# Optimization experiments

Measured on AMD Instinct MI355X. Metric: run time of the kernel, lower is better.

The kernel has to match this reference:

```python
import jax, jax.numpy as jnp
import numpy as np

BASE_C = 0.001
T = 0.7
MIN_RATIO = 0.5
MAX_RATIO = 2.0
EPS = 1e-7
BATCH, IN_DIM, HID, OUT_DIM = 65536, 784, 128, 10
WEIGHT_STD = 0.02


def _mobius_add(u, v, c):
    # (u +_c v) on the Poincare ball, last-dim vectors
    uv = jnp.sum(u * v, axis=-1, keepdims=True)
    uu = jnp.sum(u * u, axis=-1, keepdims=True)
    vv = jnp.sum(v * v, axis=-1, keepdims=True)
    num = (1.0 + 2.0 * c * uv + c * vv) * u + (1.0 - c * uu) * v
    den = 1.0 + 2.0 * c * uv + (c * c) * uu * vv
    return num / jnp.maximum(den, EPS)


def _mobius_scalar(x, c, r):
    # r (x)_c : tanh(r * artanh(sqrt(c)||x||)) * x / (sqrt(c)||x||)
    n = jnp.sqrt(jnp.maximum(jnp.sum(x * x, axis=-1, keepdims=True), EPS * EPS))
    sc = jnp.sqrt(c)
    arg = jnp.clip(sc * n, EPS, 1.0 - 1e-5)
    return jnp.tanh(r * jnp.arctanh(arg)) * x / (sc * n)


def poincare_ball_layer(h, u, c, t):
    # hyperbolic interpolation: ((1-t) (x)_c h) (+)_c (t (x)_c u)
    return _mobius_add(_mobius_scalar(h, c, 1.0 - t), _mobius_scalar(u, c, t), c)


def setup_inputs() -> dict:
    key = jax.random.key(0)
    ks = jax.random.split(key, 4)
    x = jax.random.normal(ks[0], (BATCH, IN_DIM), dtype=jnp.float32)
    weights1 = WEIGHT_STD * jax.random.normal(ks[1], (IN_DIM, HID), dtype=jnp.float32)
    bias1 = jnp.zeros((HID,), dtype=jnp.float32)
    weights2 = WEIGHT_STD * jax.random.normal(ks[2], (HID, HID), dtype=jnp.float32)
    bias2 = jnp.zeros((HID,), dtype=jnp.float32)
    out_weights = WEIGHT_STD * jax.random.normal(ks[3], (HID, OUT_DIM), dtype=jnp.float32)
    out_bias = jnp.zeros((OUT_DIM,), dtype=jnp.float32)
    curvature_scale = jnp.ones((1,), dtype=jnp.float32)
    return {"x": x, "weights1": weights1, "bias1": bias1, "weights2": weights2,
            "bias2": bias2, "out_weights": out_weights, "out_bias": out_bias,
            "curvature_scale": curvature_scale}


def reference(x, weights1, bias1, weights2, bias2, out_weights, out_bias, curvature_scale):
    x_flat = x.reshape(x.shape[0], -1)
    h = jnp.tanh(x_flat @ weights1 + bias1)            # [B, HID]
    u = jax.nn.sigmoid(h @ weights2 + bias2)           # [B, HID]
    # torch uses .item() -> curvature scale is detached from autodiff
    s = jax.lax.stop_gradient(jax.nn.sigmoid(curvature_scale[0]))
    adaptive_c = BASE_C * (MIN_RATIO + (MAX_RATIO - MIN_RATIO) * s)
    z = poincare_ball_layer(h, u, adaptive_c, T)
    z = jnp.where(jnp.any(jnp.isnan(z)), h, z)         # NaN fallback
    return z @ out_weights + out_bias
```

## Files before the change

kernel.cpp:

```cpp
#include <hip/hip_runtime.h>

typedef __attribute__((ext_vector_type(8))) short short8;
typedef __attribute__((ext_vector_type(4))) short short4v;
typedef __attribute__((ext_vector_type(4))) float f32x4;

#define BATCH 65536
#define IN_DIM 784
#define HID 128
#define OUT_DIM 10
#define KPAD 800
#define NKS 25
#define BM 128
#define NBLK (BATCH / BM)

#define OFF_W1H 0
#define OFF_W1L 204800
#define OFF_W2S 409600
#define OFF_W3S 442368

__device__ __forceinline__ unsigned short bf16_rne(float f) {
    unsigned u = __float_as_uint(f);
    return (unsigned short)((u + 0x7FFFu + ((u >> 16) & 1u)) >> 16);
}
__device__ __forceinline__ float fast_tanh(float x) {
    float e = __expf(2.0f * x);
    return 1.0f - 2.0f / (e + 1.0f);
}

__global__ void prep_kernel(const float* __restrict__ W1, const float* __restrict__ W2,
                            const float* __restrict__ W3,
                            unsigned short* __restrict__ w1h, unsigned short* __restrict__ w1l,
                            unsigned short* __restrict__ w2s, unsigned short* __restrict__ w3s) {
    int b = blockIdx.x, t = threadIdx.x;
    if (b < HID) {
        int col = b;
        for (int k = t; k < KPAD; k += 256) {
            float v = (k < IN_DIM) ? W1[k * HID + col] : 0.0f;
            unsigned u = __float_as_uint(v);
            unsigned short hi = (unsigned short)(u >> 16);
            float hif = __uint_as_float(u & 0xFFFF0000u);
            unsigned short lo = bf16_rne(v - hif);
            int idx = ((k >> 5) * HID + col) * 32 + (k & 31);
            w1h[idx] = hi; w1l[idx] = lo;
        }
    } else if (b == HID) {
        for (int i = t; i < HID * HID; i += 256) {
            int n = i >> 7, k = i & 127;
            w2s[i] = bf16_rne(W2[k * HID + n]);
        }
    } else {
        for (int i = t; i < 16 * HID; i += 256) {
            int j = i >> 7, k = i & 127;
            float v = (j < OUT_DIM) ? W3[k * OUT_DIM + j] : 0.0f;
            w3s[i] = bf16_rne(v);
        }
    }
}

__launch_bounds__(256, 2)
__global__ void fused_kernel(const float* __restrict__ X,
                             const float* __restrict__ b1,
                             const float* __restrict__ b2,
                             const float* __restrict__ ob,
                             const float* __restrict__ csc,
                             const unsigned short* __restrict__ w1h,
                             const unsigned short* __restrict__ w1l,
                             const unsigned short* __restrict__ w2s,
                             const unsigned short* __restrict__ w3s,
                             float* __restrict__ OUT) {
    __shared__ unsigned short smem[2][2][HID][40];
    unsigned short (*ht)[136] = (unsigned short (*)[136])&smem[0][0][0][0];

    const int t = threadIdx.x;
    const int wid = t >> 6, lane = t & 63;
    const int lg = lane >> 4, lr = lane & 15;
    const int row0 = blockIdx.x * BM;

    f32x4 acc[2][8];
    #pragma unroll
    for (int f = 0; f < 8; ++f) {
        float bv = b1[16 * f + lr];
        f32x4 v = {bv, bv, bv, bv};
        acc[0][f] = v; acc[1][f] = v;
    }

    f32x4 xcur[2][2], xnxt[2][2];
    short8 wcur[4], wnxt[4];

    #define LOADX(dst, ks)                                                        \
        {                                                                         \
            int k0_ = (ks) * 32 + 8 * lg;                                         \
            _Pragma("unroll")                                                     \
            for (int rf = 0; rf < 2; ++rf) {                                      \
                f32x4 a_ = {0,0,0,0}, b_ = {0,0,0,0};                             \
                if (k0_ < IN_DIM) {                                               \
                    const f32x4* p_ = (const f32x4*)(X +                          \
                        (size_t)(row0 + wid * 32 + rf * 16 + lr) * IN_DIM + k0_); \
                    a_ = p_[0]; b_ = p_[1];                                       \
                }                                                                 \
                dst[rf][0] = a_; dst[rf][1] = b_;                                 \
            }                                                                     \
        }
    #define LOADW(dst, ks)                                                        \
        {                                                                         \
            const short8* ph_ = (const short8*)(w1h + (ks) * 4096) + t * 2;       \
            const short8* pl_ = (const short8*)(w1l + (ks) * 4096) + t * 2;       \
            dst[0] = ph_[0]; dst[1] = ph_[1];                                     \
            dst[2] = pl_[0]; dst[3] = pl_[1];                                     \
        }

    LOADX(xcur, 0);
    LOADW(wcur, 0);

    for (int ks = 0; ks < NKS; ++ks) {
        const int cur = ks & 1;
        {
            short8* dh = (short8*)&smem[cur][0][t >> 1][(t & 1) * 16];
            short8* dl = (short8*)&smem[cur][1][t >> 1][(t & 1) * 16];
            dh[0] = wcur[0]; dh[1] = wcur[1];
            dl[0] = wcur[2]; dl[1] = wcur[3];
        }
        if (ks + 1 < NKS) {
            LOADX(xnxt, ks + 1);
            LOADW(wnxt, ks + 1);
        }
        __syncthreads();

        short8 xh[2], xl[2];
        #pragma unroll
        for (int rf = 0; rf < 2; ++rf) {
            short8 h8, l8;
            #pragma unroll
            for (int j = 0; j < 8; ++j) {
                float v = (j < 4) ? xcur[rf][0][j] : xcur[rf][1][j - 4];
                unsigned u = __float_as_uint(v);
                h8[j] = (short)(u >> 16);
                float lof = v - __uint_as_float(u & 0xFFFF0000u);
                l8[j] = (short)(__float_as_uint(lof) >> 16);
            }
            xh[rf] = h8; xl[rf] = l8;
        }
        #pragma unroll
        for (int f = 0; f < 8; ++f) {
            const short8 bh = *(const short8*)&smem[cur][0][16 * f + lr][8 * lg];
            const short8 bl = *(const short8*)&smem[cur][1][16 * f + lr][8 * lg];
            acc[0][f] = __builtin_amdgcn_mfma_f32_16x16x32_bf16(xh[0], bh, acc[0][f], 0, 0, 0);
            acc[1][f] = __builtin_amdgcn_mfma_f32_16x16x32_bf16(xh[1], bh, acc[1][f], 0, 0, 0);
            acc[0][f] = __builtin_amdgcn_mfma_f32_16x16x32_bf16(xl[0], bh, acc[0][f], 0, 0, 0);
            acc[1][f] = __builtin_amdgcn_mfma_f32_16x16x32_bf16(xl[1], bh, acc[1][f], 0, 0, 0);
            acc[0][f] = __builtin_amdgcn_mfma_f32_16x16x32_bf16(xh[0], bl, acc[0][f], 0, 0, 0);
            acc[1][f] = __builtin_amdgcn_mfma_f32_16x16x32_bf16(xh[1], bl, acc[1][f], 0, 0, 0);
        }
        #pragma unroll
        for (int rf = 0; rf < 2; ++rf) { xcur[rf][0] = xnxt[rf][0]; xcur[rf][1] = xnxt[rf][1]; }
        #pragma unroll
        for (int j = 0; j < 4; ++j) wcur[j] = wnxt[j];
    }
    __syncthreads();

    const float cs = csc[0];
    const float sgc = 1.0f / (1.0f + __expf(-cs));
    const float c = 0.001f * (0.5f + 1.5f * sgc);
    const float sc = sqrtf(c);

    #pragma unroll
    for (int rf = 0; rf < 2; ++rf) {
        const int rbase = wid * 32 + rf * 16 + 4 * lg;
        #pragma unroll
        for (int f = 0; f < 8; ++f) {
            short4v pk;
            #pragma unroll
            for (int r = 0; r < 4; ++r) {
                float h = fast_tanh(acc[rf][f][r]);
                acc[rf][f][r] = h;
                pk[r] = (short)bf16_rne(h);
            }
            *(short4v*)(&ht[16 * f + lr][rbase]) = pk;
        }
    }

    f32x4 uacc[2][8];
    #pragma unroll
    for (int f = 0; f < 8; ++f) {
        float bv = b2[16 * f + lr];
        f32x4 v = {bv, bv, bv, bv};
        uacc[0][f] = v; uacc[1][f] = v;
    }
    #pragma unroll
    for (int ks2 = 0; ks2 < 4; ++ks2) {
        short8 a2[2];
        #pragma unroll
        for (int rf = 0; rf < 2; ++rf) {
            const int rbl = wid * 32 + rf * 16 + lr;
            #pragma unroll
            for (int i = 0; i < 8; ++i)
                a2[rf][i] = (short)ht[ks2 * 32 + 8 * lg + i][rbl];
        }
        #pragma unroll
        for (int f = 0; f < 8; ++f) {
            const short8 bb = *(const short8*)(w2s + (16 * f + lr) * HID + ks2 * 32 + 8 * lg);
            uacc[0][f] = __builtin_amdgcn_mfma_f32_16x16x32_bf16(a2[0], bb, uacc[0][f], 0, 0, 0);
            uacc[1][f] = __builtin_amdgcn_mfma_f32_16x16x32_bf16(a2[1], bb, uacc[1][f], 0, 0, 0);
        }
    }
    #pragma unroll
    for (int rf = 0; rf < 2; ++rf)
        #pragma unroll
        for (int f = 0; f < 8; ++f)
            #pragma unroll
            for (int r = 0; r < 4; ++r)
                uacc[rf][f][r] = 1.0f / (1.0f + __expf(-uacc[rf][f][r]));

    float cA[2][4], cB[2][4];
    #pragma unroll
    for (int rf = 0; rf < 2; ++rf) {
        float hh[4] = {0,0,0,0}, uu[4] = {0,0,0,0}, hu[4] = {0,0,0,0};
        #pragma unroll
        for (int f = 0; f < 8; ++f)
            #pragma unroll
            for (int r = 0; r < 4; ++r) {
                float h = acc[rf][f][r], u = uacc[rf][f][r];
                hh[r] += h * h; uu[r] += u * u; hu[r] += h * u;
            }
        #pragma unroll
        for (int m = 1; m <= 8; m <<= 1)
            #pragma unroll
            for (int r = 0; r < 4; ++r) {
                hh[r] += __shfl_xor(hh[r], m);
                uu[r] += __shfl_xor(uu[r], m);
                hu[r] += __shfl_xor(hu[r], m);
            }
        #pragma unroll
        for (int r = 0; r < 4; ++r) {
            float nh = sqrtf(fmaxf(hh[r], 1e-14f));
            float nu = sqrtf(fmaxf(uu[r], 1e-14f));
            float argh = fminf(fmaxf(sc * nh, 1e-7f), 1.0f - 1e-5f);
            float argu = fminf(fmaxf(sc * nu, 1e-7f), 1.0f - 1e-5f);
            float ath = 0.5f * __logf((1.0f + argh) / (1.0f - argh));
            float atu = 0.5f * __logf((1.0f + argu) / (1.0f - argu));
            float alpha = fast_tanh(0.3f * ath) / (sc * nh);
            float beta  = fast_tanh(0.7f * atu) / (sc * nu);
            float UV = alpha * beta * hu[r];
            float UU = alpha * alpha * hh[r];
            float VV = beta * beta * uu[r];
            float den = fmaxf(1.0f + 2.0f * c * UV + c * c * UU * VV, 1e-7f);
            cA[rf][r] = (1.0f + 2.0f * c * UV + c * VV) * alpha / den;
            cB[rf][r] = (1.0f - c * UU) * beta / den;
        }
    }
    #pragma unroll
    for (int rf = 0; rf < 2; ++rf) {
        const int rbase = wid * 32 + rf * 16 + 4 * lg;
        #pragma unroll
        for (int f = 0; f < 8; ++f) {
            short4v pk;
            #pragma unroll
            for (int r = 0; r < 4; ++r) {
                float z = cA[rf][r] * acc[rf][f][r] + cB[rf][r] * uacc[rf][f][r];
                pk[r] = (short)bf16_rne(z);
            }
            *(short4v*)(&ht[16 * f + lr][rbase]) = pk;
        }
    }

    float obv = (lr < OUT_DIM) ? ob[lr] : 0.0f;
    f32x4 oacc[2];
    oacc[0][0] = obv; oacc[0][1] = obv; oacc[0][2] = obv; oacc[0][3] = obv;
    oacc[1] = oacc[0];
    #pragma unroll
    for (int ks2 = 0; ks2 < 4; ++ks2) {
        short8 a3[2];
        #pragma unroll
        for (int rf = 0; rf < 2; ++rf) {
            const int rbl = wid * 32 + rf * 16 + lr;
            #pragma unroll
            for (int i = 0; i < 8; ++i)
                a3[rf][i] = (short)ht[ks2 * 32 + 8 * lg + i][rbl];
        }
        const short8 b3 = *(const short8*)(w3s + lr * HID + ks2 * 32 + 8 * lg);
        oacc[0] = __builtin_amdgcn_mfma_f32_16x16x32_bf16(a3[0], b3, oacc[0], 0, 0, 0);
        oacc[1] = __builtin_amdgcn_mfma_f32_16x16x32_bf16(a3[1], b3, oacc[1], 0, 0, 0);
    }
    if (lr < OUT_DIM) {
        #pragma unroll
        for (int rf = 0; rf < 2; ++rf) {
            const int rbase = row0 + wid * 32 + rf * 16 + 4 * lg;
            #pragma unroll
            for (int r = 0; r < 4; ++r)
                OUT[(size_t)(rbase + r) * OUT_DIM + lr] = oacc[rf][r];
        }
    }
}

extern "C" void kernel_launch(void* const* d_in, const int* in_sizes, int n_in,
                              void* d_out, int out_size, void* d_ws, size_t ws_size,
                              hipStream_t stream) {
    const float* X  = (const float*)d_in[0];
    const float* W1 = (const float*)d_in[1];
    const float* B1 = (const float*)d_in[2];
    const float* W2 = (const float*)d_in[3];
    const float* B2 = (const float*)d_in[4];
    const float* W3 = (const float*)d_in[5];
    const float* OB = (const float*)d_in[6];
    const float* CS = (const float*)d_in[7];
    unsigned short* w1h = (unsigned short*)((char*)d_ws + OFF_W1H);
    unsigned short* w1l = (unsigned short*)((char*)d_ws + OFF_W1L);
    unsigned short* w2s = (unsigned short*)((char*)d_ws + OFF_W2S);
    unsigned short* w3s = (unsigned short*)((char*)d_ws + OFF_W3S);
    prep_kernel<<<HID + 2, 256, 0, stream>>>(W1, W2, W3, w1h, w1l, w2s, w3s);
    fused_kernel<<<NBLK, 256, 0, stream>>>(X, B1, B2, OB, CS, w1h, w1l, w2s, w3s, (float*)d_out);
}
```

Before: 327.5 us.

## Read W1 fragments directly from global memory instead of staging through LDS

Drops the double-buffered LDS staging of the split bf16 W1 tiles and the per-step block barrier. Each wave now loads its MFMA B fragments straight from global memory, which relies on L1/L2 caching of the small shared weight matrix. LDS use shrinks to the post-GEMM buffer and launch bounds are raised to three blocks per CU for more occupancy. The cost is more global/L1 traffic per wave, weight loads no longer prefetched one step ahead, and tighter register limits that could cause spills.

```diff
diff --git a/kernel.cpp b/kernel.cpp
--- a/kernel.cpp
+++ b/kernel.cpp
@@ -57,7 +57,7 @@
     }
 }
 
-__launch_bounds__(256, 2)
+__launch_bounds__(256, 3)
 __global__ void fused_kernel(const float* __restrict__ X,
                              const float* __restrict__ b1,
                              const float* __restrict__ b2,
@@ -68,8 +68,7 @@
                              const unsigned short* __restrict__ w2s,
                              const unsigned short* __restrict__ w3s,
                              float* __restrict__ OUT) {
-    __shared__ unsigned short smem[2][2][HID][40];
-    unsigned short (*ht)[136] = (unsigned short (*)[136])&smem[0][0][0][0];
+    __shared__ unsigned short ht[HID][136];
 
     const int t = threadIdx.x;
     const int wid = t >> 6, lane = t & 63;
@@ -85,7 +84,6 @@
     }
 
     f32x4 xcur[2][2], xnxt[2][2];
-    short8 wcur[4], wnxt[4];
 
     #define LOADX(dst, ks)                                                        \
         {                                                                         \
@@ -101,30 +99,11 @@
                 dst[rf][0] = a_; dst[rf][1] = b_;                                 \
             }                                                                     \
         }
-    #define LOADW(dst, ks)                                                        \
-        {                                                                         \
-            const short8* ph_ = (const short8*)(w1h + (ks) * 4096) + t * 2;       \
-            const short8* pl_ = (const short8*)(w1l + (ks) * 4096) + t * 2;       \
-            dst[0] = ph_[0]; dst[1] = ph_[1];                                     \
-            dst[2] = pl_[0]; dst[3] = pl_[1];                                     \
-        }
 
     LOADX(xcur, 0);
-    LOADW(wcur, 0);
 
     for (int ks = 0; ks < NKS; ++ks) {
-        const int cur = ks & 1;
-        {
-            short8* dh = (short8*)&smem[cur][0][t >> 1][(t & 1) * 16];
-            short8* dl = (short8*)&smem[cur][1][t >> 1][(t & 1) * 16];
-            dh[0] = wcur[0]; dh[1] = wcur[1];
-            dl[0] = wcur[2]; dl[1] = wcur[3];
-        }
-        if (ks + 1 < NKS) {
-            LOADX(xnxt, ks + 1);
-            LOADW(wnxt, ks + 1);
-        }
-        __syncthreads();
+        if (ks + 1 < NKS) LOADX(xnxt, ks + 1);
 
         short8 xh[2], xl[2];
         #pragma unroll
@@ -140,10 +119,13 @@
             }
             xh[rf] = h8; xl[rf] = l8;
         }
-        #pragma unroll
-        for (int f = 0; f < 8; ++f) {
-            const short8 bh = *(const short8*)&smem[cur][0][16 * f + lr][8 * lg];
-            const short8 bl = *(const short8*)&smem[cur][1][16 * f + lr][8 * lg];
+
+        const unsigned short* whp = w1h + (size_t)ks * HID * 32 + 8 * lg;
+        const unsigned short* wlp = w1l + (size_t)ks * HID * 32 + 8 * lg;
+        #pragma unroll
+        for (int f = 0; f < 8; ++f) {
+            const short8 bh = *(const short8*)(whp + (16 * f + lr) * 32);
+            const short8 bl = *(const short8*)(wlp + (16 * f + lr) * 32);
             acc[0][f] = __builtin_amdgcn_mfma_f32_16x16x32_bf16(xh[0], bh, acc[0][f], 0, 0, 0);
             acc[1][f] = __builtin_amdgcn_mfma_f32_16x16x32_bf16(xh[1], bh, acc[1][f], 0, 0, 0);
             acc[0][f] = __builtin_amdgcn_mfma_f32_16x16x32_bf16(xl[0], bh, acc[0][f], 0, 0, 0);
@@ -153,10 +135,7 @@
         }
         #pragma unroll
         for (int rf = 0; rf < 2; ++rf) { xcur[rf][0] = xnxt[rf][0]; xcur[rf][1] = xnxt[rf][1]; }
-        #pragma unroll
-        for (int j = 0; j < 4; ++j) wcur[j] = wnxt[j];
-    }
-    __syncthreads();
+    }
 
     const float cs = csc[0];
     const float sgc = 1.0f / (1.0f + __expf(-cs));
```

After: 357.2 us. +9.1%, slower.
